# Kernel tuning notes

Measured on AMD Instinct MI355X. Metric: run time of the kernel, lower is better.

## Reference

```python
import jax, jax.numpy as jnp
import numpy as np

N_HEADS = 16


def setup_inputs() -> dict:
    key = jax.random.key(0)
    ks = jax.random.split(key, 7)
    B, S, D = 2, 2048, 1024
    x = jax.random.normal(ks[0], (B, S, D), dtype=jnp.float32)
    attn_mask = jax.random.normal(ks[1], (S, S), dtype=jnp.float32) * 0.1
    attn_bias = jax.random.normal(ks[2], (B, S, S), dtype=jnp.float32) * 0.1
    Wqkv = jax.random.normal(ks[3], (D, 3 * D), dtype=jnp.float32) * (D ** -0.5)
    bqkv = jnp.zeros((3 * D,), dtype=jnp.float32)
    Wout = jax.random.normal(ks[4], (D, D), dtype=jnp.float32) * (D ** -0.5)
    bout = jnp.zeros((D,), dtype=jnp.float32)
    return {"x": x, "attn_mask": attn_mask, "attn_bias": attn_bias,
            "Wqkv": Wqkv, "bqkv": bqkv, "Wout": Wout, "bout": bout}


def reference(x, attn_mask, attn_bias, Wqkv, bqkv, Wout, bout):
    B, S, D = x.shape
    H = N_HEADS
    hd = D // H
    # qkv projection: [B,S,3D] -> [3,B,H,S,hd]
    qkv = (x @ Wqkv + bqkv).reshape(B, S, 3, H, hd).transpose(2, 0, 3, 1, 4)
    q, k, v = qkv[0], qkv[1], qkv[2]
    scores = jnp.einsum('bhqd,bhkd->bhqk', q, k) / (hd ** 0.5)
    scores = scores + attn_mask[None, None, :, :] + attn_bias[:, None, :, :]
    attn = jax.nn.softmax(scores, axis=-1)  # dropout p=0.0 (eval)
    out = jnp.einsum('bhqk,bhkd->bhqd', attn, v)
    out = out.transpose(0, 2, 1, 3).reshape(B, S, D)
    return out @ Wout + bout
```

## Files before the change

kernel.cpp:

```cpp
#include <hip/hip_runtime.h>
#include <hip/hip_bf16.h>


#define S_LEN 2048
#define DMODEL 1024
#define NH 16
#define HD 64

typedef __bf16 bf16x8 __attribute__((ext_vector_type(8)));
typedef __bf16 bf16x4 __attribute__((ext_vector_type(4)));
typedef __bf16 bf16x2v __attribute__((ext_vector_type(2)));
typedef float f32x4 __attribute__((ext_vector_type(4)));

#define GLD_LDS16(g, l)                                              \
  __builtin_amdgcn_global_load_lds(                                  \
      (const __attribute__((address_space(1))) unsigned int*)(g),    \
      (__attribute__((address_space(3))) unsigned int*)(l), 16, 0, 0)

__global__ __launch_bounds__(256) void cvt_x(const float* __restrict__ X,
                                             __bf16* __restrict__ Xb) {
  int i = blockIdx.x * 256 + threadIdx.x;
  float4 v = ((const float4*)X)[i];
  bf16x4 o = {(__bf16)v.x, (__bf16)v.y, (__bf16)v.z, (__bf16)v.w};
  *(bf16x4*)&Xb[(size_t)i * 4] = o;
}

__global__ __launch_bounds__(256) void cvt_wt(const float* __restrict__ W,
                                              __bf16* __restrict__ Wt,
                                              int ncols) {
  __shared__ float tile[64][65];
  const int n0 = blockIdx.x * 64;
  const int k0 = blockIdx.y * 64;
  const int tid = threadIdx.x;
  {
    int c = tid & 63, r4 = tid >> 6;
#pragma unroll
    for (int p = 0; p < 16; ++p) {
      int r = r4 + p * 4;
      tile[r][c] = W[(size_t)(k0 + r) * ncols + n0 + c];
    }
  }
  __syncthreads();
  {
    int cc = (tid & 31) * 2, r8 = tid >> 5;
#pragma unroll
    for (int p = 0; p < 8; ++p) {
      int rr = r8 + p * 8;
      bf16x2v o = {(__bf16)tile[cc][rr], (__bf16)tile[cc + 1][rr]};
      *(bf16x2v*)&Wt[(size_t)(n0 + rr) * 1024 + k0 + cc] = o;
    }
  }
}

__global__ __launch_bounds__(256) void mb_fuse(const float* __restrict__ mask,
                                               const float* __restrict__ bias,
                                               __bf16* __restrict__ MB) {
  const int kt = blockIdx.x, qt = blockIdx.y, b = blockIdx.z;
  const int tid = threadIdx.x;
  const int w = tid >> 6, lane = tid & 63;
  const int quad = lane >> 4, c = lane & 15;
  const int row0 = qt * 64 + w * 16 + quad * 4;
  const int col0 = kt * 64 + c;
  const float* mp = mask + (size_t)row0 * S_LEN + col0;
  const float* bp =
      bias + (size_t)b * S_LEN * S_LEN + (size_t)row0 * S_LEN + col0;
  __bf16 vals[16];
#pragma unroll
  for (int ct = 0; ct < 4; ++ct)
#pragma unroll
    for (int r = 0; r < 4; ++r)
      vals[ct * 4 + r] = (__bf16)(mp[(size_t)r * S_LEN + ct * 16] +
                                  bp[(size_t)r * S_LEN + ct * 16]);
  __bf16* op =
      MB + (((size_t)(b * 32 + qt) * 32 + kt) * 4096) + (w * 64 + lane) * 16;
  *(bf16x8*)op = *(bf16x8*)&vals[0];
  *(bf16x8*)(op + 8) = *(bf16x8*)&vals[8];
}

__global__ __launch_bounds__(256) void gemm_qkv_mfma(
    const __bf16* __restrict__ Xb, const __bf16* __restrict__ Wt,
    const float* __restrict__ bqkv, __bf16* __restrict__ Qb,
    __bf16* __restrict__ Kb, __bf16* __restrict__ Vtb) {
  __shared__ __align__(16) __bf16 As[128 * 32];
  __shared__ __align__(16) __bf16 Bs[128 * 32];
  const int tid = threadIdx.x;
  const int w = tid >> 6, lane = tid & 63;
  const int c = lane & 15, quad = lane >> 4;
  const int wm = w >> 1, wn = w & 1;
  const int rowBase = blockIdx.y * 128;
  const int colBase = blockIdx.x * 128;

  f32x4 acc[4][4] = {};

  const __bf16* gA0 =
      Xb + (size_t)(rowBase + w * 32 + (lane >> 2)) * 1024 + (lane & 3) * 8;
  const __bf16* gB0 =
      Wt + (size_t)(colBase + w * 32 + (lane >> 2)) * 1024 + (lane & 3) * 8;
  __bf16* lA0 = &As[(w * 32) * 32];
  __bf16* lB0 = &Bs[(w * 32) * 32];

  for (int k0 = 0; k0 < 1024; k0 += 32) {
    __syncthreads();
#pragma unroll
    for (int p = 0; p < 2; ++p) {
      GLD_LDS16(gA0 + (size_t)p * 16 * 1024 + k0, lA0 + p * 16 * 32);
      GLD_LDS16(gB0 + (size_t)p * 16 * 1024 + k0, lB0 + p * 16 * 32);
    }
    __syncthreads();

    bf16x8 af[4], bfr[4];
#pragma unroll
    for (int mt = 0; mt < 4; ++mt)
      af[mt] = *(const bf16x8*)&As[(wm * 64 + mt * 16 + c) * 32 + quad * 8];
#pragma unroll
    for (int nt = 0; nt < 4; ++nt)
      bfr[nt] = *(const bf16x8*)&Bs[(wn * 64 + nt * 16 + c) * 32 + quad * 8];
#pragma unroll
    for (int mt = 0; mt < 4; ++mt)
#pragma unroll
      for (int nt = 0; nt < 4; ++nt)
        acc[mt][nt] = __builtin_amdgcn_mfma_f32_16x16x32_bf16(
            af[mt], bfr[nt], acc[mt][nt], 0, 0, 0);
  }

#pragma unroll
  for (int mt = 0; mt < 4; ++mt) {
    int row0 = rowBase + wm * 64 + mt * 16 + quad * 4;
#pragma unroll
    for (int nt = 0; nt < 4; ++nt) {
      int col = colBase + wn * 64 + nt * 16 + c;
      float bias = bqkv[col];
      int three = col >> 10;
      int h = (col & 1023) >> 6;
      int d = col & 63;
#pragma unroll
      for (int r = 0; r < 4; ++r) {
        int rr = row0 + r;
        int bb = rr >> 11, s = rr & 2047;
        float val = acc[mt][nt][r] + bias;
        size_t ho = (size_t)(bb * NH + h);
        if (three == 0)
          Qb[(ho * S_LEN + s) * HD + d] = (__bf16)val;
        else if (three == 1)
          Kb[(ho * S_LEN + s) * HD + d] = (__bf16)val;
        else
          Vtb[(ho * HD + d) * S_LEN + s] = (__bf16)val;
      }
    }
  }
}

__global__ __launch_bounds__(256) void attn_mfma(
    const __bf16* __restrict__ Qb, const __bf16* __restrict__ Kb,
    const __bf16* __restrict__ Vtb, const __bf16* __restrict__ MB,
    __bf16* __restrict__ AOb) {
  const int qt = blockIdx.x, h = blockIdx.y, b = blockIdx.z;
  const int tid = threadIdx.x;
  const int w = tid >> 6;
  const int lane = tid & 63;
  const int c = lane & 15;
  const int quad = lane >> 4;

  __shared__ __align__(16) __bf16 Ks[2][64 * 64];
  __shared__ __align__(16) __bf16 Vs[2][64 * 64];
  __shared__ __align__(16) __bf16 Ps[64 * 72];

  const int qbase = qt * 64;
  const size_t headoff = (size_t)(b * NH + h) * S_LEN * HD;
  const __bf16* Qg = Qb + headoff + (size_t)qbase * HD;
  const __bf16* Kg = Kb + headoff;
  const __bf16* Vg = Vtb + headoff;
  const __bf16* MBg = MB + ((size_t)(b * 32 + qt) * 32) * 4096;

  const int f0 = tid >> 3, f1 = f0 + 32;
  const int j = tid & 7;
  const int sj0 = j ^ (f0 & 7);
  const int sj1 = j ^ (f1 & 7);
  const int lds0 = tid * 8;
  const int lds1 = (256 + tid) * 8;

  bf16x8 qa0 = *(const bf16x8*)(Qg + (w * 16 + c) * HD + quad * 8);
  bf16x8 qa1 = *(const bf16x8*)(Qg + (w * 16 + c) * HD + quad * 8 + 32);

  const int rs0 = (quad ^ (c & 7)) * 8;
  const int rs1 = ((quad + 4) ^ (c & 7)) * 8;

  f32x4 Oa[4] = {};
  float lsum[4] = {0.f, 0.f, 0.f, 0.f};

  GLD_LDS16(Kg + (size_t)f0 * HD + sj0 * 8, &Ks[0][lds0]);
  GLD_LDS16(Kg + (size_t)f1 * HD + sj1 * 8, &Ks[0][lds1]);
  GLD_LDS16(Vg + (size_t)f0 * S_LEN + sj0 * 8, &Vs[0][lds0]);
  GLD_LDS16(Vg + (size_t)f1 * S_LEN + sj1 * 8, &Vs[0][lds1]);
  __syncthreads();

  for (int kt = 0; kt < 32; ++kt) {
    const int cur = kt & 1, nxt = cur ^ 1;
    const __bf16* MBl = MBg + (size_t)kt * 4096 + (w * 64 + lane) * 16;
    bf16x8 rMB0 = *(const bf16x8*)MBl;
    bf16x8 rMB1 = *(const bf16x8*)(MBl + 8);
    if (kt < 31) {
      const int kb1 = (kt + 1) * 64;
      GLD_LDS16(Kg + (size_t)(kb1 + f0) * HD + sj0 * 8, &Ks[nxt][lds0]);
      GLD_LDS16(Kg + (size_t)(kb1 + f1) * HD + sj1 * 8, &Ks[nxt][lds1]);
      GLD_LDS16(Vg + (size_t)f0 * S_LEN + kb1 + sj0 * 8, &Vs[nxt][lds0]);
      GLD_LDS16(Vg + (size_t)f1 * S_LEN + kb1 + sj1 * 8, &Vs[nxt][lds1]);
    }

    f32x4 sv[4];
#pragma unroll
    for (int ct = 0; ct < 4; ++ct) {
      f32x4 a = {};
      bf16x8 kf0 = *(const bf16x8*)&Ks[cur][(ct * 16 + c) * 64 + rs0];
      bf16x8 kf1 = *(const bf16x8*)&Ks[cur][(ct * 16 + c) * 64 + rs1];
      a = __builtin_amdgcn_mfma_f32_16x16x32_bf16(qa0, kf0, a, 0, 0, 0);
      a = __builtin_amdgcn_mfma_f32_16x16x32_bf16(qa1, kf1, a, 0, 0, 0);
      sv[ct] = a;
    }
#pragma unroll
    for (int ct = 0; ct < 4; ++ct)
#pragma unroll
      for (int r = 0; r < 4; ++r) {
        float mb = (ct < 2) ? (float)rMB0[ct * 4 + r]
                            : (float)rMB1[(ct - 2) * 4 + r];
        float p = __expf(sv[ct][r] * 0.125f + mb - 8.0f);
        lsum[r] += p;
        Ps[(w * 16 + quad * 4 + r) * 72 + ct * 16 + c] = (__bf16)p;
      }
    bf16x8 pf0 = *(const bf16x8*)&Ps[(w * 16 + c) * 72 + quad * 8];
    bf16x8 pf1 = *(const bf16x8*)&Ps[(w * 16 + c) * 72 + quad * 8 + 32];
#pragma unroll
    for (int ft = 0; ft < 4; ++ft) {
      bf16x8 vf0 = *(const bf16x8*)&Vs[cur][(ft * 16 + c) * 64 + rs0];
      bf16x8 vf1 = *(const bf16x8*)&Vs[cur][(ft * 16 + c) * 64 + rs1];
      Oa[ft] =
          __builtin_amdgcn_mfma_f32_16x16x32_bf16(pf0, vf0, Oa[ft], 0, 0, 0);
      Oa[ft] =
          __builtin_amdgcn_mfma_f32_16x16x32_bf16(pf1, vf1, Oa[ft], 0, 0, 0);
    }

    __syncthreads();
  }
  float invl[4];
#pragma unroll
  for (int r = 0; r < 4; ++r) {
    float t = lsum[r];
    t += __shfl_xor(t, 1);
    t += __shfl_xor(t, 2);
    t += __shfl_xor(t, 4);
    t += __shfl_xor(t, 8);
    invl[r] = 1.0f / t;
  }
#pragma unroll
  for (int ft = 0; ft < 4; ++ft)
#pragma unroll
    for (int r = 0; r < 4; ++r)
      AOb[(size_t)(b * S_LEN + qbase + w * 16 + quad * 4 + r) * DMODEL +
          h * HD + ft * 16 + c] = (__bf16)(Oa[ft][r] * invl[r]);
}

__global__ __launch_bounds__(256) void gemm_out_mfma(
    const __bf16* __restrict__ AOb, const __bf16* __restrict__ Wt2,
    const float* __restrict__ bout, float* __restrict__ Out) {
  __shared__ __align__(16) __bf16 As[128 * 32];
  __shared__ __align__(16) __bf16 Bs[128 * 32];
  const int tid = threadIdx.x;
  const int w = tid >> 6, lane = tid & 63;
  const int c = lane & 15, quad = lane >> 4;
  const int wm = w >> 1, wn = w & 1;
  const int rowBase = blockIdx.y * 128;
  const int colBase = blockIdx.x * 128;

  f32x4 acc[4][4] = {};

  const __bf16* gA0 =
      AOb + (size_t)(rowBase + w * 32 + (lane >> 2)) * 1024 + (lane & 3) * 8;
  const __bf16* gB0 =
      Wt2 + (size_t)(colBase + w * 32 + (lane >> 2)) * 1024 + (lane & 3) * 8;
  __bf16* lA0 = &As[(w * 32) * 32];
  __bf16* lB0 = &Bs[(w * 32) * 32];

  for (int k0 = 0; k0 < 1024; k0 += 32) {
    __syncthreads();
#pragma unroll
    for (int p = 0; p < 2; ++p) {
      GLD_LDS16(gA0 + (size_t)p * 16 * 1024 + k0, lA0 + p * 16 * 32);
      GLD_LDS16(gB0 + (size_t)p * 16 * 1024 + k0, lB0 + p * 16 * 32);
    }
    __syncthreads();

    bf16x8 af[4], bfr[4];
#pragma unroll
    for (int mt = 0; mt < 4; ++mt)
      af[mt] = *(const bf16x8*)&As[(wm * 64 + mt * 16 + c) * 32 + quad * 8];
#pragma unroll
    for (int nt = 0; nt < 4; ++nt)
      bfr[nt] = *(const bf16x8*)&Bs[(wn * 64 + nt * 16 + c) * 32 + quad * 8];
#pragma unroll
    for (int mt = 0; mt < 4; ++mt)
#pragma unroll
      for (int nt = 0; nt < 4; ++nt)
        acc[mt][nt] = __builtin_amdgcn_mfma_f32_16x16x32_bf16(
            af[mt], bfr[nt], acc[mt][nt], 0, 0, 0);
  }

#pragma unroll
  for (int mt = 0; mt < 4; ++mt) {
    int row0 = rowBase + wm * 64 + mt * 16 + quad * 4;
#pragma unroll
    for (int nt = 0; nt < 4; ++nt) {
      int col = colBase + wn * 64 + nt * 16 + c;
      float bias = bout[col];
#pragma unroll
      for (int r = 0; r < 4; ++r)
        Out[(size_t)(row0 + r) * 1024 + col] = acc[mt][nt][r] + bias;
    }
  }
}

extern "C" void kernel_launch(void* const* d_in, const int* in_sizes, int n_in,
                              void* d_out, int out_size, void* d_ws,
                              size_t ws_size, hipStream_t stream) {
  const float* x = (const float*)d_in[0];
  const float* attn_mask = (const float*)d_in[1];
  const float* attn_bias = (const float*)d_in[2];
  const float* Wqkv = (const float*)d_in[3];
  const float* bqkv = (const float*)d_in[4];
  const float* Wout = (const float*)d_in[5];
  const float* bout = (const float*)d_in[6];
  float* out = (float*)d_out;

  __bf16* base = (__bf16*)d_ws;
  __bf16* Xb = base;
  __bf16* AOb = base;
  __bf16* Wt = base + 4194304;
  __bf16* Qb = base + 8388608;
  __bf16* Kb = base + 12582912;
  __bf16* Vtb = base + 16777216;
  __bf16* MB = base + 20971520;
  __bf16* Wt2 = base + 29360128;

  cvt_x<<<4096, 256, 0, stream>>>(x, Xb);
  cvt_wt<<<dim3(48, 16), 256, 0, stream>>>(Wqkv, Wt, 3072);
  cvt_wt<<<dim3(16, 16), 256, 0, stream>>>(Wout, Wt2, 1024);
  mb_fuse<<<dim3(32, 32, 2), 256, 0, stream>>>(attn_mask, attn_bias, MB);
  gemm_qkv_mfma<<<dim3(24, 32), 256, 0, stream>>>(Xb, Wt, bqkv, Qb, Kb, Vtb);
  attn_mfma<<<dim3(32, NH, 2), 256, 0, stream>>>(Qb, Kb, Vtb, MB, AOb);
  gemm_out_mfma<<<dim3(8, 32), 256, 0, stream>>>(AOb, Wt2, bout, out);
}
```

Before: 309.9 us.

## Transpose attention score layout to keep P in registers and skip LDS round-trip

Swaps MFMA operand order so each lane holds a query row's scores across keys. The softmax probabilities can then feed the PV product directly from registers via 16x16x16 bf16 MFMAs, removing the LDS write/read of P. The fused mask/bias kernel now reads with float4 loads in the matching transposed layout, and the output store and row-sum reduction become vectorized and cheaper. The cost is twice as many smaller MFMAs and 8-byte V fragment loads, plus a fallback path through a per-wave LDS buffer when the builtin is missing.

```diff
diff --git a/kernel.cpp b/kernel.cpp
--- a/kernel.cpp
+++ b/kernel.cpp
@@ -11,11 +11,18 @@
 typedef __bf16 bf16x4 __attribute__((ext_vector_type(4)));
 typedef __bf16 bf16x2v __attribute__((ext_vector_type(2)));
 typedef float f32x4 __attribute__((ext_vector_type(4)));
+typedef short s16x4 __attribute__((ext_vector_type(4)));
 
 #define GLD_LDS16(g, l)                                              \
   __builtin_amdgcn_global_load_lds(                                  \
       (const __attribute__((address_space(1))) unsigned int*)(g),    \
       (__attribute__((address_space(3))) unsigned int*)(l), 16, 0, 0)
+
+#if __has_builtin(__builtin_amdgcn_mfma_f32_16x16x16bf16_1k)
+#define HAVE_MFMA_16x16x16_BF16 1
+#else
+#define HAVE_MFMA_16x16x16_BF16 0
+#endif
 
 __global__ __launch_bounds__(256) void cvt_x(const float* __restrict__ X,
                                              __bf16* __restrict__ Xb) {
@@ -59,18 +66,20 @@
   const int tid = threadIdx.x;
   const int w = tid >> 6, lane = tid & 63;
   const int quad = lane >> 4, c = lane & 15;
-  const int row0 = qt * 64 + w * 16 + quad * 4;
-  const int col0 = kt * 64 + c;
-  const float* mp = mask + (size_t)row0 * S_LEN + col0;
-  const float* bp =
-      bias + (size_t)b * S_LEN * S_LEN + (size_t)row0 * S_LEN + col0;
+  const size_t qrow = (size_t)(qt * 64 + w * 16 + c);
+  const int col0 = kt * 64 + quad * 4;
+  const float* mp = mask + qrow * S_LEN + col0;
+  const float* bp = bias + (size_t)b * S_LEN * S_LEN + qrow * S_LEN + col0;
   __bf16 vals[16];
 #pragma unroll
-  for (int ct = 0; ct < 4; ++ct)
-#pragma unroll
-    for (int r = 0; r < 4; ++r)
-      vals[ct * 4 + r] = (__bf16)(mp[(size_t)r * S_LEN + ct * 16] +
-                                  bp[(size_t)r * S_LEN + ct * 16]);
+  for (int ct = 0; ct < 4; ++ct) {
+    float4 m = *(const float4*)(mp + ct * 16);
+    float4 a = *(const float4*)(bp + ct * 16);
+    vals[ct * 4 + 0] = (__bf16)(m.x + a.x);
+    vals[ct * 4 + 1] = (__bf16)(m.y + a.y);
+    vals[ct * 4 + 2] = (__bf16)(m.z + a.z);
+    vals[ct * 4 + 3] = (__bf16)(m.w + a.w);
+  }
   __bf16* op =
       MB + (((size_t)(b * 32 + qt) * 32 + kt) * 4096) + (w * 64 + lane) * 16;
   *(bf16x8*)op = *(bf16x8*)&vals[0];
@@ -163,7 +172,9 @@
 
   __shared__ __align__(16) __bf16 Ks[2][64 * 64];
   __shared__ __align__(16) __bf16 Vs[2][64 * 64];
-  __shared__ __align__(16) __bf16 Ps[64 * 72];
+#if !HAVE_MFMA_16x16x16_BF16
+  __shared__ __align__(16) __bf16 P2[4][16 * 72];
+#endif
 
   const int qbase = qt * 64;
   const size_t headoff = (size_t)(b * NH + h) * S_LEN * HD;
@@ -186,7 +197,7 @@
   const int rs1 = ((quad + 4) ^ (c & 7)) * 8;
 
   f32x4 Oa[4] = {};
-  float lsum[4] = {0.f, 0.f, 0.f, 0.f};
+  float lsum = 0.f;
 
   GLD_LDS16(Kg + (size_t)f0 * HD + sj0 * 8, &Ks[0][lds0]);
   GLD_LDS16(Kg + (size_t)f1 * HD + sj1 * 8, &Ks[0][lds1]);
@@ -213,50 +224,70 @@
       f32x4 a = {};
       bf16x8 kf0 = *(const bf16x8*)&Ks[cur][(ct * 16 + c) * 64 + rs0];
       bf16x8 kf1 = *(const bf16x8*)&Ks[cur][(ct * 16 + c) * 64 + rs1];
-      a = __builtin_amdgcn_mfma_f32_16x16x32_bf16(qa0, kf0, a, 0, 0, 0);
-      a = __builtin_amdgcn_mfma_f32_16x16x32_bf16(qa1, kf1, a, 0, 0, 0);
+      a = __builtin_amdgcn_mfma_f32_16x16x32_bf16(kf0, qa0, a, 0, 0, 0);
+      a = __builtin_amdgcn_mfma_f32_16x16x32_bf16(kf1, qa1, a, 0, 0, 0);
       sv[ct] = a;
     }
-#pragma unroll
-    for (int ct = 0; ct < 4; ++ct)
+    s16x4 pb[4];
+#pragma unroll
+    for (int ct = 0; ct < 4; ++ct) {
+      __bf16 t4[4];
 #pragma unroll
       for (int r = 0; r < 4; ++r) {
         float mb = (ct < 2) ? (float)rMB0[ct * 4 + r]
                             : (float)rMB1[(ct - 2) * 4 + r];
         float p = __expf(sv[ct][r] * 0.125f + mb - 8.0f);
-        lsum[r] += p;
-        Ps[(w * 16 + quad * 4 + r) * 72 + ct * 16 + c] = (__bf16)p;
+        lsum += p;
+        t4[r] = (__bf16)p;
       }
-    bf16x8 pf0 = *(const bf16x8*)&Ps[(w * 16 + c) * 72 + quad * 8];
-    bf16x8 pf1 = *(const bf16x8*)&Ps[(w * 16 + c) * 72 + quad * 8 + 32];
+      pb[ct] = *(s16x4*)t4;
+    }
+
+#if HAVE_MFMA_16x16x16_BF16
 #pragma unroll
     for (int ft = 0; ft < 4; ++ft) {
-      bf16x8 vf0 = *(const bf16x8*)&Vs[cur][(ft * 16 + c) * 64 + rs0];
-      bf16x8 vf1 = *(const bf16x8*)&Vs[cur][(ft * 16 + c) * 64 + rs1];
+      const int fr = ft * 16 + c;
+#pragma unroll
+      for (int ct = 0; ct < 4; ++ct) {
+        const int chunk = ((ct * 2 + (quad >> 1)) ^ (fr & 7)) * 8 +
+                          (quad & 1) * 4;
+        s16x4 vf = *(const s16x4*)&Vs[cur][fr * 64 + chunk];
+        Oa[ft] = __builtin_amdgcn_mfma_f32_16x16x16bf16_1k(vf, pb[ct],
+                                                           Oa[ft], 0, 0, 0);
+      }
+    }
+#else
+#pragma unroll
+    for (int ct = 0; ct < 4; ++ct)
+      *(bf16x4*)&P2[w][c * 72 + ct * 16 + quad * 4] = *(bf16x4*)&pb[ct];
+    bf16x8 pf0 = *(const bf16x8*)&P2[w][c * 72 + quad * 8];
+    bf16x8 pf1 = *(const bf16x8*)&P2[w][c * 72 + 32 + quad * 8];
+#pragma unroll
+    for (int ft = 0; ft < 4; ++ft) {
+      const int fr = ft * 16 + c;
+      bf16x8 vf0 = *(const bf16x8*)&Vs[cur][fr * 64 + rs0];
+      bf16x8 vf1 = *(const bf16x8*)&Vs[cur][fr * 64 + rs1];
       Oa[ft] =
-          __builtin_amdgcn_mfma_f32_16x16x32_bf16(pf0, vf0, Oa[ft], 0, 0, 0);
+          __builtin_amdgcn_mfma_f32_16x16x32_bf16(vf0, pf0, Oa[ft], 0, 0, 0);
       Oa[ft] =
-          __builtin_amdgcn_mfma_f32_16x16x32_bf16(pf1, vf1, Oa[ft], 0, 0, 0);
-    }
-
-    __syncthreads();
-  }
-  float invl[4];
-#pragma unroll
-  for (int r = 0; r < 4; ++r) {
-    float t = lsum[r];
-    t += __shfl_xor(t, 1);
-    t += __shfl_xor(t, 2);
-    t += __shfl_xor(t, 4);
-    t += __shfl_xor(t, 8);
-    invl[r] = 1.0f / t;
-  }
-#pragma unroll
-  for (int ft = 0; ft < 4; ++ft)
-#pragma unroll
-    for (int r = 0; r < 4; ++r)
-      AOb[(size_t)(b * S_LEN + qbase + w * 16 + quad * 4 + r) * DMODEL +
-          h * HD + ft * 16 + c] = (__bf16)(Oa[ft][r] * invl[r]);
+          __builtin_amdgcn_mfma_f32_16x16x32_bf16(vf1, pf1, Oa[ft], 0, 0, 0);
+    }
+#endif
+
+    __syncthreads();
+  }
+  lsum += __shfl_xor(lsum, 16);
+  lsum += __shfl_xor(lsum, 32);
+  const float invl = 1.0f / lsum;
+  __bf16* orow =
+      AOb + (size_t)(b * S_LEN + qbase + w * 16 + c) * DMODEL + h * HD;
+#pragma unroll
+  for (int ft = 0; ft < 4; ++ft) {
+    __bf16 t4[4];
+#pragma unroll
+    for (int r = 0; r < 4; ++r) t4[r] = (__bf16)(Oa[ft][r] * invl);
+    *(bf16x4*)(orow + ft * 16 + quad * 4) = *(bf16x4*)t4;
+  }
 }
 
 __global__ __launch_bounds__(256) void gemm_out_mfma(
```

New measurement: 283.2 us. -8.6%, faster.
